# Kernel tuning notes

Measured on AMD Instinct MI355X. Metric: run time of the kernel, lower is better.

## Reference

```python
import jax, jax.numpy as jnp
import numpy as np
from jax.scipy.special import logsumexp

B, T, V, E, H, L = 64, 256, 50000, 256, 256, 9


def setup_inputs() -> dict:
    key = jax.random.key(0)
    ks = jax.random.split(key, 10)
    lengths = jax.random.randint(ks[0], (B,), T // 2, T + 1)
    pm = jnp.arange(T)[None, :] < lengths[:, None]  # valid-token mask, padding at tail
    inp = jnp.where(pm, jax.random.randint(ks[1], (B, T), 1, V), 0).astype(jnp.int32)
    tags = jnp.where(pm, jax.random.randint(ks[2], (B, T), 0, L), 0).astype(jnp.int32)
    s = 0.05
    emb = jax.random.normal(ks[3], (V, E)) * s
    Wf = jax.random.normal(ks[4], (E, 4 * H)) * s
    Uf = jax.random.normal(ks[5], (H, 4 * H)) * s
    bf = jnp.zeros((4 * H,))
    Wb = jax.random.normal(ks[6], (E, 4 * H)) * s
    Ub = jax.random.normal(ks[7], (H, 4 * H)) * s
    bb = jnp.zeros((4 * H,))
    Wd = jax.random.normal(ks[8], (2 * H, L)) * s
    bd = jnp.zeros((L,))
    trans = jax.random.uniform(ks[9], (L, L))
    return dict(inp=inp, tags=tags, emb=emb, Wf=Wf, Uf=Uf, bf=bf,
                Wb=Wb, Ub=Ub, bb=bb, Wd=Wd, bd=bd, trans=trans)


def _lstm(x, mask, W, U, b):
    """Keras-style LSTM with masking (state + output carried through masked steps).
    x: [B,T,E], mask: [B,T] bool -> [B,T,H]."""
    h0 = jnp.zeros((x.shape[0], H), x.dtype)
    c0 = h0

    def step(carry, xm):
        h, c = carry
        xt, mt = xm
        z = xt @ W + h @ U + b  # [B,4H], gate order i,f,g,o (Keras)
        i, f, g, o = jnp.split(z, 4, axis=-1)
        c_new = jax.nn.sigmoid(f) * c + jax.nn.sigmoid(i) * jnp.tanh(g)
        h_new = jax.nn.sigmoid(o) * jnp.tanh(c_new)
        m = mt[:, None]
        h = jnp.where(m, h_new, h)
        c = jnp.where(m, c_new, c)
        return (h, c), h

    _, hs = jax.lax.scan(step, (h0, c0), (x.transpose(1, 0, 2), mask.T))
    return hs.transpose(1, 0, 2)


def _crf_log_likelihood(pot, tags, seq_lens, trans):
    """tfa.text.crf_log_likelihood: sequence_score - log_norm. pot: [B,T,L]."""
    Bv, Tv, Lv = pot.shape
    tmask = (jnp.arange(Tv)[None, :] < seq_lens[:, None]).astype(pot.dtype)
    unary = jnp.sum(jnp.take_along_axis(pot, tags[..., None], axis=-1)[..., 0] * tmask, axis=1)
    pmask = (jnp.arange(Tv - 1)[None, :] < (seq_lens - 1)[:, None]).astype(pot.dtype)
    binary = jnp.sum(trans[tags[:, :-1], tags[:, 1:]] * pmask, axis=1)

    # forward algorithm; alpha frozen once t >= seq_len (tfa uses dynamic_rnn semantics)
    def step(carry, pot_t):
        alpha, t = carry
        new = pot_t + logsumexp(alpha[:, :, None] + trans[None], axis=1)  # [B,L]
        alpha = jnp.where((t < seq_lens)[:, None], new, alpha)
        return (alpha, t + 1), None

    (alpha, _), _ = jax.lax.scan(step, (pot[:, 0, :], jnp.int32(1)),
                                 pot[:, 1:].transpose(1, 0, 2))
    log_norm = logsumexp(alpha, axis=-1)
    return unary + binary - log_norm


def reference(inp, tags, emb, Wf, Uf, bf, Wb, Ub, bb, Wd, bd, trans):
    mask = inp != 0
    seq_lens = jnp.sum(mask.astype(jnp.int32), axis=-1)
    x = jnp.take(emb, inp, axis=0)  # [B,T,E]; dropout is identity (inference)
    hf = _lstm(x, mask, Wf, Uf, bf)
    hb = _lstm(x[:, ::-1], mask[:, ::-1], Wb, Ub, bb)[:, ::-1]
    pot = jnp.concatenate([hf, hb], axis=-1) @ Wd + bd  # [B,T,L]
    ll = _crf_log_likelihood(pot, tags, seq_lens, trans)
    loss = -jnp.mean(ll / seq_lens.astype(pot.dtype))
    return pot, seq_lens, loss
```

## Files before the change

kernel.cpp:

```cpp
#include <hip/hip_runtime.h>

#define B_ 64
#define T_ 256
#define E_ 256
#define H_ 256
#define G4 1024
#define L_ 9

typedef __attribute__((ext_vector_type(8))) short bf16x8;
typedef __attribute__((ext_vector_type(4))) float f32x4;
typedef _Float16 half2v __attribute__((ext_vector_type(2)));

__device__ __forceinline__ ushort f2bf(float x){
  unsigned u = __float_as_uint(x);
  unsigned r = (u + 0x7FFFu + ((u >> 16) & 1u)) >> 16;
  return (ushort)r;
}
__device__ __forceinline__ float bf2f(unsigned u16v){
  return __uint_as_float(u16v << 16);
}
__device__ __forceinline__ float fsig(float x){
  return __builtin_amdgcn_rcpf(1.f + __expf(-x));
}
__device__ __forceinline__ float ftanh(float x){
  return 1.f - 2.f * __builtin_amdgcn_rcpf(__expf(2.f * x) + 1.f);
}
__device__ __forceinline__ int sdot4(unsigned a, unsigned b, int c){
#if __has_builtin(__builtin_amdgcn_sdot4)
  return __builtin_amdgcn_sdot4((int)a, (int)b, c, false);
#else
  int r = c;
  #pragma unroll
  for (int j = 0; j < 4; j++){
    int av = (int)(signed char)((a >> (8 * j)) & 0xFF);
    int bv = (int)(signed char)((b >> (8 * j)) & 0xFF);
    r += av * bv;
  }
  return r;
#endif
}

__global__ void k_prep(const int* __restrict__ inp, const float* __restrict__ emb,
                       const float* __restrict__ Wf, const float* __restrict__ Wb,
                       const float* __restrict__ Uf, const float* __restrict__ Ub,
                       ushort* __restrict__ WT, unsigned* __restrict__ Uq,
                       float* __restrict__ su, ushort* __restrict__ X,
                       int* __restrict__ lens, float* __restrict__ out_len){
  int bid = blockIdx.x, tid = threadIdx.x;
  if (bid < 2048){
    int idx = bid * 256 + tid;
    int dir = idx >> 18; int rem = idx & 262143;
    int n = rem >> 8, k = rem & 255;
    const float* W = dir ? Wb : Wf;
    WT[idx] = f2bf(W[k * G4 + n]);
  } else if (bid < 4096){
    int idx = bid - 2048;
    int dir = idx >> 10, cc = idx & 1023;
    const float* U = dir ? Ub : Uf;
    float v = U[tid * G4 + cc];
    __shared__ float red[4];
    __shared__ float ssu;
    __shared__ char qb[256];
    float a = fabsf(v);
    #pragma unroll
    for (int off = 32; off; off >>= 1) a = fmaxf(a, __shfl_xor(a, off));
    int lane = tid & 63, w = tid >> 6;
    if (lane == 0) red[w] = a;
    __syncthreads();
    if (tid == 0){
      float m = fmaxf(fmaxf(red[0], red[1]), fmaxf(red[2], red[3]));
      float s = fmaxf(m, 1e-20f) * (1.f / 127.f);
      ssu = s;
      su[idx] = s;
    }
    __syncthreads();
    float s = ssu;
    int q = __float2int_rn(v / s);
    q = max(-127, min(127, q));
    qb[tid] = (char)q;
    __syncthreads();
    if (tid < 64)
      Uq[dir * 65536 + tid * 1024 + cc] = *(const unsigned*)&qb[tid * 4];
  } else if (bid < 6144){
    int idx = (bid - 4096) * 256 + tid;
    int m = idx >> 5, koff = (idx & 31) * 8;
    int tok = inp[m];
    const float* src = emb + (size_t)tok * E_ + koff;
    float4 a = *(const float4*)src;
    float4 b = *(const float4*)(src + 4);
    uint4 o;
    o.x = (unsigned)f2bf(a.x) | ((unsigned)f2bf(a.y) << 16);
    o.y = (unsigned)f2bf(a.z) | ((unsigned)f2bf(a.w) << 16);
    o.z = (unsigned)f2bf(b.x) | ((unsigned)f2bf(b.y) << 16);
    o.w = (unsigned)f2bf(b.z) | ((unsigned)f2bf(b.w) << 16);
    *(uint4*)(X + m * E_ + koff) = o;
  } else {
    int w = tid >> 6, lane = tid & 63;
    int b = (bid - 6144) * 4 + w;
    int c = 0;
    for (int t = lane; t < T_; t += 64) c += (inp[b * T_ + t] != 0);
    for (int off = 32; off; off >>= 1) c += __shfl_xor(c, off);
    if (lane == 0){ lens[b] = c; out_len[b] = (float)c; }
  }
}

__global__ __launch_bounds__(256) void k_gemm(const ushort* __restrict__ X,
        const ushort* __restrict__ WT, const float* __restrict__ bf_,
        const float* __restrict__ bb_, ushort* __restrict__ Zpf, ushort* __restrict__ Zpb){
  int zi = blockIdx.z;
  const ushort* wt = WT + zi * 262144;
  const float* bias = zi ? bb_ : bf_;
  ushort* Zp = zi ? Zpb : Zpf;
  int m0 = blockIdx.x * 128, n0 = blockIdx.y * 128;
  __shared__ ushort As[128][40];
  __shared__ ushort Bs[128][40];
  int tid = threadIdx.x;
  int sr = tid >> 1, sk = (tid & 1) * 16;
  const ushort* xg = X + (m0 + sr) * E_ + sk;
  const ushort* wg = wt + (n0 + sr) * E_ + sk;
  f32x4 acc[4][4] = {};
  int lane = tid & 63, wv = tid >> 6;
  int wr = wv >> 1, wc = wv & 1;
  int lrow = lane & 15, kf = (lane >> 4) * 8;
  for (int k0 = 0; k0 < E_; k0 += 32){
    uint4 a0 = *(const uint4*)(xg + k0);
    uint4 a1 = *(const uint4*)(xg + k0 + 8);
    uint4 b0 = *(const uint4*)(wg + k0);
    uint4 b1 = *(const uint4*)(wg + k0 + 8);
    *(uint4*)&As[sr][sk]     = a0;  *(uint4*)&As[sr][sk + 8] = a1;
    *(uint4*)&Bs[sr][sk]     = b0;  *(uint4*)&Bs[sr][sk + 8] = b1;
    __syncthreads();
    bf16x8 af[4], bfr[4];
    #pragma unroll
    for (int i = 0; i < 4; i++) af[i]  = *(const bf16x8*)&As[wr * 64 + i * 16 + lrow][kf];
    #pragma unroll
    for (int i = 0; i < 4; i++) bfr[i] = *(const bf16x8*)&Bs[wc * 64 + i * 16 + lrow][kf];
    #pragma unroll
    for (int i = 0; i < 4; i++)
      #pragma unroll
      for (int j = 0; j < 4; j++)
        acc[i][j] = __builtin_amdgcn_mfma_f32_16x16x32_bf16(af[i], bfr[j], acc[i][j], 0, 0, 0);
    __syncthreads();
  }
  int crow = (lane >> 4) * 4;
  #pragma unroll
  for (int j = 0; j < 4; j++){
    int col = n0 + wc * 64 + j * 16 + lrow;
    float bv = bias[col];
    int gg = col >> 8, jj = col & 255;
    #pragma unroll
    for (int i = 0; i < 4; i++){
      int rbase = m0 + wr * 64 + i * 16 + crow;
      #pragma unroll
      for (int r = 0; r < 4; r++)
        Zp[((size_t)(rbase + r) * 256 + jj) * 4 + gg] = f2bf(acc[i][j][r] + bv);
    }
  }
}

__global__ __launch_bounds__(1024, 4) void k_recur8(
    const ushort* __restrict__ Zpf, const ushort* __restrict__ Zpb,
    const unsigned* __restrict__ Uq, const float* __restrict__ su,
    const int* __restrict__ lens, ushort* __restrict__ hf16, ushort* __restrict__ hb16){
  int bid = blockIdx.x;
  int dir = bid >> 6, b = bid & 63;
  const uint2* Zp = (const uint2*)(dir ? Zpb : Zpf);
  ushort* H = dir ? hb16 : hf16;
  const unsigned* Uqd = Uq + dir * 65536;
  int tid = threadIdx.x;
  float sc = su[dir * 1024 + tid] * (1.f / 127.f);
  int alen = lens[b];

  unsigned uq[64];
  {
    const unsigned* p = Uqd + tid;
    #pragma unroll
    for (int i = 0; i < 64; i++){
      asm volatile("global_load_dword %0, %1, off" : "=v"(uq[i]) : "v"(p));
      p += 1024;
    }
    asm volatile("s_waitcnt vmcnt(0)" ::: "memory");
    __builtin_amdgcn_sched_barrier(0);
  }

  __shared__ float zsh[1024];
  __shared__ unsigned hq[2][64];

  if (tid < 64){ hq[0][tid] = 0u; }
  __syncthreads();

  float c_st = 0.f, h_st = 0.f;
  int t0 = dir ? 255 : 0;
  uint2 zw = uint2{0u, 0u};
  if (tid < 256) zw = Zp[(size_t)(b * 256 + t0) * 256 + tid];

  for (int s_ = 0; s_ < 256; ++s_){
    int t = dir ? (255 - s_) : s_;
    int tn = dir ? (t - 1) : (t + 1);
    int cur = s_ & 1, nxt = cur ^ 1;
    uint2 zw_n = uint2{0u, 0u};
    if (tid < 256 && s_ < 255) zw_n = Zp[(size_t)(b * 256 + tn) * 256 + tid];
    int acc0 = 0, acc1 = 0;
    const uint4* hp = (const uint4*)hq[cur];
    #pragma unroll
    for (int i = 0; i < 16; i++){
      uint4 hv = hp[i];
      acc0 = sdot4(uq[4 * i + 0], hv.x, acc0);
      acc1 = sdot4(uq[4 * i + 1], hv.y, acc1);
      acc0 = sdot4(uq[4 * i + 2], hv.z, acc0);
      acc1 = sdot4(uq[4 * i + 3], hv.w, acc1);
    }
    zsh[tid] = (float)(acc0 + acc1) * sc;
    __syncthreads();
    if (tid < 256){
      float zi = bf2f(zw.x & 0xffffu) + zsh[tid];
      float zf = bf2f(zw.x >> 16)     + zsh[256 + tid];
      float zg = bf2f(zw.y & 0xffffu) + zsh[512 + tid];
      float zo = bf2f(zw.y >> 16)     + zsh[768 + tid];
      if (t < alen){
        c_st = fsig(zf) * c_st + fsig(zi) * ftanh(zg);
        h_st = fsig(zo) * ftanh(c_st);
      }
      int ri = __float2int_rn(h_st * 127.f);
      ((char*)hq[nxt])[tid] = (char)ri;
      unsigned hw = f2bf(h_st);
      unsigned other = (unsigned)__shfl_xor((int)hw, 1);
      if (!(tid & 1)){
        unsigned word = hw | (other << 16);
        *(unsigned*)&H[(size_t)(b * 256 + t) * H_ + tid] = word;
      }
    }
    __syncthreads();
    zw = zw_n;
  }
}

__global__ __launch_bounds__(256) void k_pot(const ushort* __restrict__ hf16,
        const ushort* __restrict__ hb16, const float* __restrict__ Wd,
        const float* __restrict__ bd, float* __restrict__ out, int* __restrict__ cnt){
  if (blockIdx.x == 0 && threadIdx.x == 0) *cnt = 0;
  int lane = threadIdx.x & 63, wid = threadIdx.x >> 6;
  int m = blockIdx.x * 4 + wid;
  uint2 ua = *(const uint2*)&hf16[(size_t)m * H_ + lane * 4];
  uint2 ub = *(const uint2*)&hb16[(size_t)m * H_ + lane * 4];
  float av[4] = {bf2f(ua.x & 0xFFFFu), bf2f(ua.x >> 16), bf2f(ua.y & 0xFFFFu), bf2f(ua.y >> 16)};
  float bv[4] = {bf2f(ub.x & 0xFFFFu), bf2f(ub.x >> 16), bf2f(ub.y & 0xFFFFu), bf2f(ub.y >> 16)};
  float acc[9];
  #pragma unroll
  for (int l = 0; l < 9; l++) acc[l] = 0.f;
  #pragma unroll
  for (int i = 0; i < 4; i++){
    int r = lane * 4 + i;
    #pragma unroll
    for (int l = 0; l < 9; l++)
      acc[l] += av[i] * Wd[r * 9 + l] + bv[i] * Wd[(H_ + r) * 9 + l];
  }
  #pragma unroll
  for (int off = 32; off; off >>= 1)
    #pragma unroll
    for (int l = 0; l < 9; l++) acc[l] += __shfl_xor(acc[l], off);
  if (lane == 0){
    #pragma unroll
    for (int l = 0; l < 9; l++) out[(size_t)m * 9 + l] = acc[l] + bd[l];
  }
}

__global__ void k_post(const float* __restrict__ out, const int* __restrict__ tags,
                       const float* __restrict__ trans, const int* __restrict__ lens,
                       float* __restrict__ lln, int* cnt, float* __restrict__ loss_out){
  int b = blockIdx.x, lane = threadIdx.x;
  int len = lens[b];
  const float* pot = out + (size_t)b * T_ * 9;
  float up = 0.f, bp = 0.f;
  for (int t = lane; t < T_; t += 64){
    int tg = tags[b * T_ + t];
    if (t < len) up += pot[t * 9 + tg];
    if (t + 1 < len){
      int tg2 = tags[b * T_ + t + 1];
      bp += trans[tg * 9 + tg2];
    }
  }
  for (int off = 32; off; off >>= 1){ up += __shfl_xor(up, off); bp += __shfl_xor(bp, off); }
  float alpha = 0.f;
  if (lane < 9){
    float tr[9];
    #pragma unroll
    for (int i = 0; i < 9; i++) tr[i] = trans[i * 9 + lane];
    alpha = pot[lane];
    for (int t = 1; t < T_; ++t){
      float v[9];
      #pragma unroll
      for (int i = 0; i < 9; i++) v[i] = __shfl(alpha, i) + tr[i];
      float mx = v[0];
      #pragma unroll
      for (int i = 1; i < 9; i++) mx = fmaxf(mx, v[i]);
      float sum = 0.f;
      #pragma unroll
      for (int i = 0; i < 9; i++) sum += __expf(v[i] - mx);
      float an = pot[t * 9 + lane] + mx + __logf(sum);
      if (t < len) alpha = an;
    }
  }
  float mx2 = -3.4e38f;
  for (int i = 0; i < 9; i++){ float a = __shfl(alpha, i); mx2 = fmaxf(mx2, a); }
  float s2 = 0.f;
  for (int i = 0; i < 9; i++){ float a = __shfl(alpha, i); s2 += __expf(a - mx2); }
  float lse = mx2 + __logf(s2);
  __shared__ int lastf;
  if (lane == 0){
    __hip_atomic_store(&lln[b], (up + bp - lse) / (float)len,
                       __ATOMIC_RELAXED, __HIP_MEMORY_SCOPE_AGENT);
    int old = __hip_atomic_fetch_add(cnt, 1, __ATOMIC_ACQ_REL, __HIP_MEMORY_SCOPE_AGENT);
    lastf = (old == 63);
  }
  __syncthreads();
  if (lastf){
    float v = __hip_atomic_load(&lln[lane], __ATOMIC_RELAXED, __HIP_MEMORY_SCOPE_AGENT);
    for (int off = 32; off; off >>= 1) v += __shfl_xor(v, off);
    if (lane == 0) loss_out[0] = -v * (1.f / 64.f);
  }
}

extern "C" void kernel_launch(void* const* d_in, const int* in_sizes, int n_in,
                              void* d_out, int out_size, void* d_ws, size_t ws_size,
                              hipStream_t stream) {
  (void)in_sizes; (void)n_in; (void)out_size; (void)ws_size;
  const int*   inp   = (const int*)  d_in[0];
  const int*   tags  = (const int*)  d_in[1];
  const float* emb   = (const float*)d_in[2];
  const float* Wf    = (const float*)d_in[3];
  const float* Uf    = (const float*)d_in[4];
  const float* bfv   = (const float*)d_in[5];
  const float* Wb    = (const float*)d_in[6];
  const float* Ub    = (const float*)d_in[7];
  const float* bbv   = (const float*)d_in[8];
  const float* Wd    = (const float*)d_in[9];
  const float* bd    = (const float*)d_in[10];
  const float* trans = (const float*)d_in[11];
  float* out = (float*)d_out;

  char* ws = (char*)d_ws;
  unsigned* Uq   = (unsigned*)(ws);
  float*    su   = (float*)   (ws + 524288);
  ushort*   WT16 = (ushort*)  (ws + 1048576);
  ushort*   Xbf  = (ushort*)  (ws + 2097152);
  int*      cnt  = (int*)     (ws + 2097152);
  ushort*   Zpf  = (ushort*)  (ws + 10485760);
  ushort*   Zpb  = (ushort*)  (ws + 44040192);
  ushort*   hf16 = (ushort*)  (ws + 77594624);
  ushort*   hb16 = (ushort*)  (ws + 85983232);
  int*      lens = (int*)     (ws + 94371840);
  float*    lln  = (float*)   (ws + 94372096);

  k_prep<<<6160, 256, 0, stream>>>(inp, emb, Wf, Wb, Uf, Ub, WT16, Uq, su, Xbf,
                                   lens, out + 147456);
  k_gemm<<<dim3(128, 8, 2), 256, 0, stream>>>(Xbf, WT16, bfv, bbv, Zpf, Zpb);
  k_recur8<<<128, 1024, 0, stream>>>(Zpf, Zpb, Uq, su, lens, hf16, hb16);
  k_pot<<<4096, 256, 0, stream>>>(hf16, hb16, Wd, bd, out, cnt);
  k_post<<<64, 64, 0, stream>>>(out, tags, trans, lens, lln, cnt, out + 147520);
}
```

Measured before the change: 417.6 us.

## Halve recurrence block size, each thread computes two gate columns with vector loads

The LSTM recurrence kernel now runs 512 threads per block instead of 1024, with each thread holding quantized U weights for two gate columns and accumulating both dot products. The Uq layout is transposed to column-major so each thread can load its weights with 16-byte vector loads. This aims to cut per-step barrier cost and LDS broadcast reads of h by reusing each h load for two columns. In exchange, register pressure per thread doubles, and only 256 of the 512 threads do the gate math, so the share of threads idle during that phase rises.

```diff
diff --git a/kernel.cpp b/kernel.cpp
--- a/kernel.cpp
+++ b/kernel.cpp
@@ -9,6 +9,7 @@
 
 typedef __attribute__((ext_vector_type(8))) short bf16x8;
 typedef __attribute__((ext_vector_type(4))) float f32x4;
+typedef __attribute__((ext_vector_type(4))) unsigned uint4v;
 typedef _Float16 half2v __attribute__((ext_vector_type(2)));
 
 __device__ __forceinline__ ushort f2bf(float x){
@@ -80,7 +81,7 @@
     qb[tid] = (char)q;
     __syncthreads();
     if (tid < 64)
-      Uq[dir * 65536 + tid * 1024 + cc] = *(const unsigned*)&qb[tid * 4];
+      Uq[dir * 65536 + cc * 64 + tid] = *(const unsigned*)&qb[tid * 4];
   } else if (bid < 6144){
     int idx = (bid - 4096) * 256 + tid;
     int m = idx >> 5, koff = (idx & 31) * 8;
@@ -158,7 +159,7 @@
   }
 }
 
-__global__ __launch_bounds__(1024, 4) void k_recur8(
+__global__ __launch_bounds__(512, 2) void k_recur9(
     const ushort* __restrict__ Zpf, const ushort* __restrict__ Zpb,
     const unsigned* __restrict__ Uq, const float* __restrict__ su,
     const int* __restrict__ lens, ushort* __restrict__ hf16, ushort* __restrict__ hb16){
@@ -168,16 +169,19 @@
   ushort* H = dir ? hb16 : hf16;
   const unsigned* Uqd = Uq + dir * 65536;
   int tid = threadIdx.x;
-  float sc = su[dir * 1024 + tid] * (1.f / 127.f);
+  int c0 = tid, c1 = tid + 512;
+  float scA = su[dir * 1024 + c0] * (1.f / 127.f);
+  float scB = su[dir * 1024 + c1] * (1.f / 127.f);
   int alen = lens[b];
 
-  unsigned uq[64];
+  uint4v uqA[16], uqB[16];
   {
-    const unsigned* p = Uqd + tid;
-    #pragma unroll
-    for (int i = 0; i < 64; i++){
-      asm volatile("global_load_dword %0, %1, off" : "=v"(uq[i]) : "v"(p));
-      p += 1024;
+    const unsigned* pa = Uqd + c0 * 64;
+    const unsigned* pb = Uqd + c1 * 64;
+    #pragma unroll
+    for (int i = 0; i < 16; i++){
+      asm volatile("global_load_dwordx4 %0, %1, off" : "=v"(uqA[i]) : "v"(pa + 4 * i));
+      asm volatile("global_load_dwordx4 %0, %1, off" : "=v"(uqB[i]) : "v"(pb + 4 * i));
     }
     asm volatile("s_waitcnt vmcnt(0)" ::: "memory");
     __builtin_amdgcn_sched_barrier(0);
@@ -200,17 +204,22 @@
     int cur = s_ & 1, nxt = cur ^ 1;
     uint2 zw_n = uint2{0u, 0u};
     if (tid < 256 && s_ < 255) zw_n = Zp[(size_t)(b * 256 + tn) * 256 + tid];
-    int acc0 = 0, acc1 = 0;
+    int aA0 = 0, aA1 = 0, aB0 = 0, aB1 = 0;
     const uint4* hp = (const uint4*)hq[cur];
     #pragma unroll
     for (int i = 0; i < 16; i++){
       uint4 hv = hp[i];
-      acc0 = sdot4(uq[4 * i + 0], hv.x, acc0);
-      acc1 = sdot4(uq[4 * i + 1], hv.y, acc1);
-      acc0 = sdot4(uq[4 * i + 2], hv.z, acc0);
-      acc1 = sdot4(uq[4 * i + 3], hv.w, acc1);
-    }
-    zsh[tid] = (float)(acc0 + acc1) * sc;
+      aA0 = sdot4(uqA[i][0], hv.x, aA0);
+      aA1 = sdot4(uqA[i][1], hv.y, aA1);
+      aB0 = sdot4(uqB[i][0], hv.x, aB0);
+      aB1 = sdot4(uqB[i][1], hv.y, aB1);
+      aA0 = sdot4(uqA[i][2], hv.z, aA0);
+      aA1 = sdot4(uqA[i][3], hv.w, aA1);
+      aB0 = sdot4(uqB[i][2], hv.z, aB0);
+      aB1 = sdot4(uqB[i][3], hv.w, aB1);
+    }
+    zsh[c0] = (float)(aA0 + aA1) * scA;
+    zsh[c1] = (float)(aB0 + aB1) * scB;
     __syncthreads();
     if (tid < 256){
       float zi = bf2f(zw.x & 0xffffu) + zsh[tid];
@@ -355,7 +364,7 @@
   k_prep<<<6160, 256, 0, stream>>>(inp, emb, Wf, Wb, Uf, Ub, WT16, Uq, su, Xbf,
                                    lens, out + 147456);
   k_gemm<<<dim3(128, 8, 2), 256, 0, stream>>>(Xbf, WT16, bfv, bbv, Zpf, Zpb);
-  k_recur8<<<128, 1024, 0, stream>>>(Zpf, Zpb, Uq, su, lens, hf16, hb16);
+  k_recur9<<<128, 512, 0, stream>>>(Zpf, Zpb, Uq, su, lens, hf16, hb16);
   k_pot<<<4096, 256, 0, stream>>>(hf16, hb16, Wd, bd, out, cnt);
   k_post<<<64, 64, 0, stream>>>(out, tags, trans, lens, lln, cnt, out + 147520);
 }
```

After: 408.7 us. 1.02x faster.

## Remap LSTM recurrence so each thread pair owns all four gates of a unit

Applied to the files above, without the earlier changes.

The recurrence kernel now uses 512 threads per sequence, with each pair of threads splitting the K dimension of one hidden unit and computing all four gate dot products. Partial sums are combined with a lane shuffle. This removes the shared-memory gate exchange and one of the two block barriers per timestep. The int8 U matrix is repacked in the prep kernel so each thread can load its weights with dwordx4 loads. The cost is heavier per-thread register use (128 dwords of weights) and the gate nonlinearities being computed redundantly by both threads of each pair.

```diff
diff --git a/kernel.cpp b/kernel.cpp
--- a/kernel.cpp
+++ b/kernel.cpp
@@ -9,6 +9,7 @@
 
 typedef __attribute__((ext_vector_type(8))) short bf16x8;
 typedef __attribute__((ext_vector_type(4))) float f32x4;
+typedef __attribute__((ext_vector_type(4))) unsigned uint4v;
 typedef _Float16 half2v __attribute__((ext_vector_type(2)));
 
 __device__ __forceinline__ ushort f2bf(float x){
@@ -56,6 +57,7 @@
   } else if (bid < 4096){
     int idx = bid - 2048;
     int dir = idx >> 10, cc = idx & 1023;
+    int u = cc & 255, g = cc >> 8;
     const float* U = dir ? Ub : Uf;
     float v = U[tid * G4 + cc];
     __shared__ float red[4];
@@ -79,8 +81,11 @@
     q = max(-127, min(127, q));
     qb[tid] = (char)q;
     __syncthreads();
-    if (tid < 64)
-      Uq[dir * 65536 + tid * 1024 + cc] = *(const unsigned*)&qb[tid * 4];
+    if (tid < 64){
+      int khalf = tid >> 5, kk = tid & 31;
+      Uq[dir * 65536 + u * 256 + khalf * 128 + g * 32 + kk] =
+          *(const unsigned*)&qb[tid * 4];
+    }
   } else if (bid < 6144){
     int idx = (bid - 4096) * 256 + tid;
     int m = idx >> 5, koff = (idx & 31) * 8;
@@ -158,7 +163,7 @@
   }
 }
 
-__global__ __launch_bounds__(1024, 4) void k_recur8(
+__global__ __launch_bounds__(512, 2) void k_recur10(
     const ushort* __restrict__ Zpf, const ushort* __restrict__ Zpb,
     const unsigned* __restrict__ Uq, const float* __restrict__ su,
     const int* __restrict__ lens, ushort* __restrict__ hf16, ushort* __restrict__ hb16){
@@ -166,69 +171,71 @@
   int dir = bid >> 6, b = bid & 63;
   const uint2* Zp = (const uint2*)(dir ? Zpb : Zpf);
   ushort* H = dir ? hb16 : hf16;
-  const unsigned* Uqd = Uq + dir * 65536;
   int tid = threadIdx.x;
-  float sc = su[dir * 1024 + tid] * (1.f / 127.f);
+  int u = tid >> 1, khalf = tid & 1;
+  float sc0 = su[dir * 1024 +        u] * (1.f / 127.f);
+  float sc1 = su[dir * 1024 + 256 +  u] * (1.f / 127.f);
+  float sc2 = su[dir * 1024 + 512 +  u] * (1.f / 127.f);
+  float sc3 = su[dir * 1024 + 768 +  u] * (1.f / 127.f);
   int alen = lens[b];
 
-  unsigned uq[64];
+  uint4v uq[4][8];
   {
-    const unsigned* p = Uqd + tid;
-    #pragma unroll
-    for (int i = 0; i < 64; i++){
-      asm volatile("global_load_dword %0, %1, off" : "=v"(uq[i]) : "v"(p));
-      p += 1024;
-    }
+    const unsigned* p = Uq + dir * 65536 + u * 256 + khalf * 128;
+    #pragma unroll
+    for (int g = 0; g < 4; g++)
+      #pragma unroll
+      for (int i = 0; i < 8; i++)
+        asm volatile("global_load_dwordx4 %0, %1, off"
+                     : "=v"(uq[g][i]) : "v"(p + g * 32 + i * 4));
     asm volatile("s_waitcnt vmcnt(0)" ::: "memory");
     __builtin_amdgcn_sched_barrier(0);
   }
 
-  __shared__ float zsh[1024];
   __shared__ unsigned hq[2][64];
-
-  if (tid < 64){ hq[0][tid] = 0u; }
+  if (tid < 128) ((unsigned*)hq)[tid] = 0u;
   __syncthreads();
 
   float c_st = 0.f, h_st = 0.f;
   int t0 = dir ? 255 : 0;
-  uint2 zw = uint2{0u, 0u};
-  if (tid < 256) zw = Zp[(size_t)(b * 256 + t0) * 256 + tid];
+  uint2 zw = Zp[(size_t)(b * 256 + t0) * 256 + u];
 
   for (int s_ = 0; s_ < 256; ++s_){
     int t = dir ? (255 - s_) : s_;
     int tn = dir ? (t - 1) : (t + 1);
     int cur = s_ & 1, nxt = cur ^ 1;
     uint2 zw_n = uint2{0u, 0u};
-    if (tid < 256 && s_ < 255) zw_n = Zp[(size_t)(b * 256 + tn) * 256 + tid];
-    int acc0 = 0, acc1 = 0;
-    const uint4* hp = (const uint4*)hq[cur];
-    #pragma unroll
-    for (int i = 0; i < 16; i++){
+    if (s_ < 255) zw_n = Zp[(size_t)(b * 256 + tn) * 256 + u];
+    int a0 = 0, a1 = 0, a2 = 0, a3 = 0;
+    const uint4* hp = (const uint4*)&hq[cur][khalf * 32];
+    #pragma unroll
+    for (int i = 0; i < 8; i++){
       uint4 hv = hp[i];
-      acc0 = sdot4(uq[4 * i + 0], hv.x, acc0);
-      acc1 = sdot4(uq[4 * i + 1], hv.y, acc1);
-      acc0 = sdot4(uq[4 * i + 2], hv.z, acc0);
-      acc1 = sdot4(uq[4 * i + 3], hv.w, acc1);
-    }
-    zsh[tid] = (float)(acc0 + acc1) * sc;
-    __syncthreads();
-    if (tid < 256){
-      float zi = bf2f(zw.x & 0xffffu) + zsh[tid];
-      float zf = bf2f(zw.x >> 16)     + zsh[256 + tid];
-      float zg = bf2f(zw.y & 0xffffu) + zsh[512 + tid];
-      float zo = bf2f(zw.y >> 16)     + zsh[768 + tid];
-      if (t < alen){
-        c_st = fsig(zf) * c_st + fsig(zi) * ftanh(zg);
-        h_st = fsig(zo) * ftanh(c_st);
-      }
+      a0 = sdot4(uq[0][i][0], hv.x, a0);  a0 = sdot4(uq[0][i][1], hv.y, a0);
+      a0 = sdot4(uq[0][i][2], hv.z, a0);  a0 = sdot4(uq[0][i][3], hv.w, a0);
+      a1 = sdot4(uq[1][i][0], hv.x, a1);  a1 = sdot4(uq[1][i][1], hv.y, a1);
+      a1 = sdot4(uq[1][i][2], hv.z, a1);  a1 = sdot4(uq[1][i][3], hv.w, a1);
+      a2 = sdot4(uq[2][i][0], hv.x, a2);  a2 = sdot4(uq[2][i][1], hv.y, a2);
+      a2 = sdot4(uq[2][i][2], hv.z, a2);  a2 = sdot4(uq[2][i][3], hv.w, a2);
+      a3 = sdot4(uq[3][i][0], hv.x, a3);  a3 = sdot4(uq[3][i][1], hv.y, a3);
+      a3 = sdot4(uq[3][i][2], hv.z, a3);  a3 = sdot4(uq[3][i][3], hv.w, a3);
+    }
+    a0 += __shfl_xor(a0, 1);
+    a1 += __shfl_xor(a1, 1);
+    a2 += __shfl_xor(a2, 1);
+    a3 += __shfl_xor(a3, 1);
+    float zi = bf2f(zw.x & 0xffffu) + (float)a0 * sc0;
+    float zf = bf2f(zw.x >> 16)     + (float)a1 * sc1;
+    float zg = bf2f(zw.y & 0xffffu) + (float)a2 * sc2;
+    float zo = bf2f(zw.y >> 16)     + (float)a3 * sc3;
+    if (t < alen){
+      c_st = fsig(zf) * c_st + fsig(zi) * ftanh(zg);
+      h_st = fsig(zo) * ftanh(c_st);
+    }
+    if (khalf == 0){
       int ri = __float2int_rn(h_st * 127.f);
-      ((char*)hq[nxt])[tid] = (char)ri;
-      unsigned hw = f2bf(h_st);
-      unsigned other = (unsigned)__shfl_xor((int)hw, 1);
-      if (!(tid & 1)){
-        unsigned word = hw | (other << 16);
-        *(unsigned*)&H[(size_t)(b * 256 + t) * H_ + tid] = word;
-      }
+      ((char*)hq[nxt])[u] = (char)ri;
+      H[(size_t)(b * 256 + t) * H_ + u] = f2bf(h_st);
     }
     __syncthreads();
     zw = zw_n;
@@ -355,7 +362,7 @@
   k_prep<<<6160, 256, 0, stream>>>(inp, emb, Wf, Wb, Uf, Ub, WT16, Uq, su, Xbf,
                                    lens, out + 147456);
   k_gemm<<<dim3(128, 8, 2), 256, 0, stream>>>(Xbf, WT16, bfv, bbv, Zpf, Zpb);
-  k_recur8<<<128, 1024, 0, stream>>>(Zpf, Zpb, Uq, su, lens, hf16, hb16);
+  k_recur10<<<128, 512, 0, stream>>>(Zpf, Zpb, Uq, su, lens, hf16, hb16);
   k_pot<<<4096, 256, 0, stream>>>(hf16, hb16, Wd, bd, out, cnt);
   k_post<<<64, 64, 0, stream>>>(out, tags, trans, lens, lln, cnt, out + 147520);
 }
```

After: 410.5 us. About the same (-1.7%).
